# Performance work log

Hardware: AMD Instinct MI355X
Metric: run time of the kernel (lower is better)

The kernel has to match this reference:

```python
import jax, jax.numpy as jnp
import numpy as np

G, NP, K, H, DH, D, NL = 256, 1000, 8, 8, 10, 80, 10  # graphs, nodes/graph, knn, heads, d_head, hidden, layers


def setup_inputs() -> dict:
    key = jax.random.key(0)
    ks = jax.random.split(key, 16)
    rn = lambda k, shape: (jax.random.normal(k, shape, jnp.float32) * 0.05)
    return dict(
        h_feat=jax.random.normal(ks[0], (G, NP, 9), jnp.float32),
        bn_gamma=jnp.ones((9,), jnp.float32), bn_beta=jnp.zeros((9,), jnp.float32),
        W_emb=rn(ks[1], (9, D)), b_emb=jnp.zeros((D,), jnp.float32),
        Wq=rn(ks[2], (NL, D, D)), Wk=rn(ks[3], (NL, D, D)), Wv=rn(ks[4], (NL, D, D)),
        Wo=rn(ks[5], (NL, D, D)), bo=jnp.zeros((NL, D), jnp.float32),
        W1=rn(ks[6], (NL, D, 2 * D)), b1=jnp.zeros((NL, 2 * D), jnp.float32),
        W2=rn(ks[7], (NL, 2 * D, D)), b2=jnp.zeros((NL, D), jnp.float32),
        Wr0=rn(ks[8], (D, 40)), br0=jnp.zeros((40,), jnp.float32),
        Wr1=rn(ks[9], (40, 20)), br1=jnp.zeros((20,), jnp.float32),
        Wr2=rn(ks[10], (20, 64)), br2=jnp.zeros((64,), jnp.float32),
        W_clust=rn(ks[11], (64, 3)),
        W_beta=rn(ks[12], (64, 1)), b_beta=jnp.zeros((1,), jnp.float32),
    )


def _forward(h_feat, bn_gamma, bn_beta, W_emb, b_emb, Wq, Wk, Wv, Wo, bo,
             W1, b1, W2, b2, Wr0, br0, Wr1, br1, Wr2, br2, W_clust, W_beta, b_beta):
    # knn graph on raw coords (first 3 feature columns), per graph, k=8 (self included)
    coords = h_feat[..., :3]
    d2 = jnp.sum((coords[:, :, None, :] - coords[:, None, :, :]) ** 2, -1)  # [G,NP,NP]
    nbr = jax.lax.top_k(-d2, K)[1]  # [G,NP,K] neighbor indices per destination node
    gidx = jnp.arange(G)[:, None, None]

    # BatchNorm1d (training-mode batch stats over all nodes) + embedding
    x = h_feat.reshape(-1, 9)
    mu = x.mean(0)
    var = x.var(0)
    x = (x - mu) / jnp.sqrt(var + 1e-5) * bn_gamma + bn_beta
    h = (x @ W_emb + b_emb).reshape(G, NP, D)

    inv_sqrt_d = jnp.float32(1.0 / np.sqrt(DH))

    def layer(h, p):
        wq, wk, wv, wo, bo_, w1, b1_, w2, b2_ = p
        q = (h @ wq).reshape(G, NP, H, DH)
        k_ = (h @ wk).reshape(G, NP, H, DH)
        v = (h @ wv).reshape(G, NP, H, DH)
        kn = k_[gidx, nbr]  # [G,NP,K,H,DH] gather src K over edges
        vn = v[gidx, nbr]
        s = jnp.einsum('gnkhd,gnhd->gnkh', kn, q) * inv_sqrt_d
        s = jnp.exp(jnp.clip(s, -5.0, 5.0))  # scaled_exp with clamp
        wV = jnp.einsum('gnkh,gnkhd->gnhd', s, vn)
        attn = (wV / (s.sum(2)[..., None] + 1e-6)).reshape(G, NP, D)
        h = h + attn @ wo + bo_  # O proj + residual (no LN/BN)
        h = h + jax.nn.relu(h @ w1 + b1_) @ w2 + b2_  # FFN + residual
        return h, None

    h, _ = jax.lax.scan(layer, h, (Wq, Wk, Wv, Wo, bo, W1, b1, W2, b2))

    # MLPReadout 80->40->20->64 (ReLU between), then clustering coords + beta
    y = h.reshape(-1, D)
    y = jax.nn.relu(y @ Wr0 + br0)
    y = jax.nn.relu(y @ Wr1 + br1)
    y = y @ Wr2 + br2
    cc = y @ W_clust  # [N,3], no bias
    beta = y @ W_beta + b_beta  # [N,1]
    return jnp.concatenate([cc, beta], axis=1)  # [N,4]


def reference(h_feat, bn_gamma, bn_beta, W_emb, b_emb, Wq, Wk, Wv, Wo, bo,
              W1, b1, W2, b2, Wr0, br0, Wr1, br1, Wr2, br2, W_clust, W_beta, b_beta):
    return _forward(h_feat, bn_gamma, bn_beta, W_emb, b_emb, Wq, Wk, Wv, Wo, bo,
                    W1, b1, W2, b2, Wr0, br0, Wr1, br1, Wr2, br2, W_clust, W_beta, b_beta)
```

## Files before the change

### kernel.cpp

```cpp
#include <hip/hip_runtime.h>
#include <cstdint>
#include <cstddef>


typedef __attribute__((ext_vector_type(8))) short short8v;
typedef __attribute__((ext_vector_type(4))) float f32x4;

#define MFMA16(ACC, A, B) ACC = __builtin_amdgcn_mfma_f32_16x16x32_bf16(A, B, ACC, 0, 0, 0)
#define MF3(ACC, AH, AL, BH, BL) { MFMA16(ACC, AH, BH); MFMA16(ACC, AH, BL); MFMA16(ACC, AL, BH); }

__device__ __forceinline__ void splitbf(float x, unsigned short& hi, unsigned short& lo) {
  unsigned u = __float_as_uint(x);
  unsigned r = u + 0x7FFFu + ((u >> 16) & 1u);
  hi = (unsigned short)(r >> 16);
  float hf = __uint_as_float(((unsigned)hi) << 16);
  float lf = x - hf;
  unsigned u2 = __float_as_uint(lf);
  unsigned r2 = u2 + 0x7FFFu + ((u2 >> 16) & 1u);
  lo = (unsigned short)(r2 >> 16);
}

__device__ __forceinline__ float bf2f(unsigned short v) {
  return __uint_as_float(((unsigned)v) << 16);
}

__global__ __launch_bounds__(128) void knn_kernel(const float* __restrict__ hf, int* __restrict__ nbr) {
  __shared__ __align__(16) float cs[3000];
  int b = blockIdx.x;
  int g = b >> 3;
  int q = b & 7;
  for (int i = threadIdx.x; i < 3000; i += 128) {
    cs[i] = hf[((size_t)g * 1000 + (i / 3)) * 9 + (i % 3)];
  }
  __syncthreads();
  int tid = threadIdx.x;
  if (tid < 125) {
    int n = q * 125 + tid;
    float cx = cs[n * 3 + 0], cy = cs[n * 3 + 1], cz = cs[n * 3 + 2];
    float bd[8];
    int bi[8];
    #pragma unroll
    for (int q2 = 0; q2 < 8; ++q2) { bd[q2] = 3.402823466e38f; bi[q2] = 0; }
    for (int j = 0; j < 1000; j += 4) {
      float4 a = *reinterpret_cast<const float4*>(cs + j * 3);
      float4 b4 = *reinterpret_cast<const float4*>(cs + j * 3 + 4);
      float4 c4 = *reinterpret_cast<const float4*>(cs + j * 3 + 8);
      float d2v[4];
      {
        float dx = __fsub_rn(cx, a.x), dy = __fsub_rn(cy, a.y), dz = __fsub_rn(cz, a.z);
        d2v[0] = __fadd_rn(__fadd_rn(__fmul_rn(dx, dx), __fmul_rn(dy, dy)), __fmul_rn(dz, dz));
      }
      {
        float dx = __fsub_rn(cx, a.w), dy = __fsub_rn(cy, b4.x), dz = __fsub_rn(cz, b4.y);
        d2v[1] = __fadd_rn(__fadd_rn(__fmul_rn(dx, dx), __fmul_rn(dy, dy)), __fmul_rn(dz, dz));
      }
      {
        float dx = __fsub_rn(cx, b4.z), dy = __fsub_rn(cy, b4.w), dz = __fsub_rn(cz, c4.x);
        d2v[2] = __fadd_rn(__fadd_rn(__fmul_rn(dx, dx), __fmul_rn(dy, dy)), __fmul_rn(dz, dz));
      }
      {
        float dx = __fsub_rn(cx, c4.y), dy = __fsub_rn(cy, c4.z), dz = __fsub_rn(cz, c4.w);
        d2v[3] = __fadd_rn(__fadd_rn(__fmul_rn(dx, dx), __fmul_rn(dy, dy)), __fmul_rn(dz, dz));
      }
      #pragma unroll
      for (int u = 0; u < 4; ++u) {
        float d2 = d2v[u];
        if (d2 < bd[7]) {
          bd[7] = d2; bi[7] = j + u;
          #pragma unroll
          for (int q2 = 7; q2 >= 1; --q2) {
            if (bd[q2] < bd[q2 - 1]) {
              float tf = bd[q2]; bd[q2] = bd[q2 - 1]; bd[q2 - 1] = tf;
              int ti = bi[q2]; bi[q2] = bi[q2 - 1]; bi[q2 - 1] = ti;
            }
          }
        }
      }
    }
    #pragma unroll
    for (int kk = 0; kk < 8; ++kk) nbr[((size_t)g * 1000 + n) * 8 + kk] = bi[kk];
  }
}

__global__ __launch_bounds__(256) void bn_stat1(const float* __restrict__ hf, float* __restrict__ partial) {
  __shared__ float red[4][18];
  int row = blockIdx.x * 256 + threadIdx.x;
  float s[9], ss[9];
  #pragma unroll
  for (int f = 0; f < 9; ++f) {
    float v = hf[(size_t)row * 9 + f];
    s[f] = v;
    ss[f] = v * v;
  }
  for (int off = 32; off > 0; off >>= 1) {
    #pragma unroll
    for (int f = 0; f < 9; ++f) {
      s[f] += __shfl_down(s[f], off);
      ss[f] += __shfl_down(ss[f], off);
    }
  }
  int wid = threadIdx.x >> 6, lane = threadIdx.x & 63;
  if (lane == 0) {
    #pragma unroll
    for (int f = 0; f < 9; ++f) { red[wid][f] = s[f]; red[wid][9 + f] = ss[f]; }
  }
  __syncthreads();
  if (threadIdx.x < 18) {
    partial[(size_t)blockIdx.x * 18 + threadIdx.x] =
        red[0][threadIdx.x] + red[1][threadIdx.x] + red[2][threadIdx.x] + red[3][threadIdx.x];
  }
}

__global__ __launch_bounds__(256) void bn_stat2(const float* __restrict__ partial, float* __restrict__ stats) {
  __shared__ double sd[9][28], qd[9][28];
  int tid = threadIdx.x;
  if (tid < 252) {
    int f = tid % 9, gq = tid / 9;
    double s = 0.0, q = 0.0;
    for (int b = gq; b < 1000; b += 28) {
      s += (double)partial[b * 18 + f];
      q += (double)partial[b * 18 + 9 + f];
    }
    sd[f][gq] = s;
    qd[f][gq] = q;
  }
  __syncthreads();
  if (tid < 9) {
    double s = 0.0, q = 0.0;
    for (int g2 = 0; g2 < 28; ++g2) { s += sd[tid][g2]; q += qd[tid][g2]; }
    double mu = s / 256000.0;
    double var = q / 256000.0 - mu * mu;
    stats[tid] = (float)mu;
    stats[9 + tid] = (float)(1.0 / sqrt(var + 1e-5));
  }
}

__global__ __launch_bounds__(256) void split_tr(const float* __restrict__ src, unsigned short* __restrict__ dhi,
                                                unsigned short* __restrict__ dlo, int R, int C, int KS) {
  const float* s = src + (size_t)blockIdx.x * R * C;
  unsigned short* dh = dhi + (size_t)blockIdx.x * C * KS;
  unsigned short* dl = dlo + (size_t)blockIdx.x * C * KS;
  int n = C * KS;
  for (int i = threadIdx.x; i < n; i += 256) {
    int c = i / KS, kk = i % KS;
    float v = (kk < R) ? s[kk * C + c] : 0.f;
    unsigned short h, l;
    splitbf(v, h, l);
    dh[i] = h;
    dl[i] = l;
  }
}

__global__ __launch_bounds__(320) void embed_kernel(const float* __restrict__ hf, const float* __restrict__ stats,
                                                    const float* __restrict__ gamma, const float* __restrict__ beta,
                                                    const float* __restrict__ We, const float* __restrict__ be,
                                                    float* __restrict__ h) {
  __shared__ __align__(16) float xs[40 * 9];
  size_t p0 = (size_t)blockIdx.x * 40;
  for (int i = threadIdx.x; i < 360; i += 320) {
    int f = i % 9;
    float x = hf[p0 * 9 + i];
    xs[i] = (x - stats[f]) * stats[9 + f] * gamma[f] + beta[f];
  }
  __syncthreads();
  int c = threadIdx.x % 80, pg = threadIdx.x / 80;
  float we[9];
  #pragma unroll
  for (int f = 0; f < 9; ++f) we[f] = We[f * 80 + c];
  float bias = be[c];
  for (int pp = 0; pp < 10; ++pp) {
    int p = pg * 10 + pp;
    float acc = 0.f;
    #pragma unroll
    for (int f = 0; f < 9; ++f) acc = fmaf(xs[p * 9 + f], we[f], acc);
    h[(p0 + p) * 80 + c] = acc + bias;
  }
}

__global__ __launch_bounds__(320) void kv_kernel(const float* __restrict__ h,
                                                 const unsigned short* __restrict__ WkH, const unsigned short* __restrict__ WkL,
                                                 const unsigned short* __restrict__ WvH, const unsigned short* __restrict__ WvL,
                                                 float* __restrict__ kb, float* __restrict__ vb) {
  __shared__ __align__(16) unsigned short ahi[48 * 104];
  __shared__ __align__(16) unsigned short alo[48 * 104];
  size_t p0 = (size_t)blockIdx.x * 40;
  int tid = threadIdx.x;
  int lane = tid & 63, wv = tid >> 6;
  int fr = lane & 15, fq = lane >> 4;
  for (int i = tid; i < 800; i += 320) {
    int row = i / 20, kq = i % 20;
    float4 v = reinterpret_cast<const float4*>(h + (p0 + row) * 80)[kq];
    unsigned short h0, l0, h1, l1, h2, l2, h3, l3;
    splitbf(v.x, h0, l0); splitbf(v.y, h1, l1); splitbf(v.z, h2, l2); splitbf(v.w, h3, l3);
    int off = row * 104 + kq * 4;
    *reinterpret_cast<unsigned*>(&ahi[off]) = (unsigned)h0 | ((unsigned)h1 << 16);
    *reinterpret_cast<unsigned*>(&ahi[off + 2]) = (unsigned)h2 | ((unsigned)h3 << 16);
    *reinterpret_cast<unsigned*>(&alo[off]) = (unsigned)l0 | ((unsigned)l1 << 16);
    *reinterpret_cast<unsigned*>(&alo[off + 2]) = (unsigned)l2 | ((unsigned)l3 << 16);
  }
  for (int i = tid; i < 384; i += 320) {
    int row = i >> 3, kk = 80 + ((i & 7) << 1);
    int off = row * 104 + kk;
    *reinterpret_cast<unsigned*>(&ahi[off]) = 0u;
    *reinterpret_cast<unsigned*>(&alo[off]) = 0u;
  }
  __syncthreads();
  int bcol = wv * 16 + fr;
  f32x4 ck0 = {0.f, 0.f, 0.f, 0.f}, ck1 = ck0, ck2 = ck0;
  f32x4 cv0 = ck0, cv1 = ck0, cv2 = ck0;
  #pragma unroll
  for (int ks = 0; ks < 3; ++ks) {
    int boff = bcol * 96 + ks * 32 + fq * 8;
    short8v bkh = *reinterpret_cast<const short8v*>(WkH + boff);
    short8v bkl = *reinterpret_cast<const short8v*>(WkL + boff);
    short8v bvh = *reinterpret_cast<const short8v*>(WvH + boff);
    short8v bvl = *reinterpret_cast<const short8v*>(WvL + boff);
    int a0 = (0 * 16 + fr) * 104 + ks * 32 + fq * 8;
    int a1 = (1 * 16 + fr) * 104 + ks * 32 + fq * 8;
    int a2 = (2 * 16 + fr) * 104 + ks * 32 + fq * 8;
    short8v ah0 = *reinterpret_cast<const short8v*>(ahi + a0);
    short8v al0 = *reinterpret_cast<const short8v*>(alo + a0);
    MF3(ck0, ah0, al0, bkh, bkl); MF3(cv0, ah0, al0, bvh, bvl);
    short8v ah1 = *reinterpret_cast<const short8v*>(ahi + a1);
    short8v al1 = *reinterpret_cast<const short8v*>(alo + a1);
    MF3(ck1, ah1, al1, bkh, bkl); MF3(cv1, ah1, al1, bvh, bvl);
    short8v ah2 = *reinterpret_cast<const short8v*>(ahi + a2);
    short8v al2 = *reinterpret_cast<const short8v*>(alo + a2);
    MF3(ck2, ah2, al2, bkh, bkl); MF3(cv2, ah2, al2, bvh, bvl);
  }
  #pragma unroll
  for (int j = 0; j < 4; ++j) {
    int r0 = fq * 4 + j;
    kb[(p0 + r0) * 80 + bcol] = ck0[j];
    vb[(p0 + r0) * 80 + bcol] = cv0[j];
    int r1 = 16 + r0;
    kb[(p0 + r1) * 80 + bcol] = ck1[j];
    vb[(p0 + r1) * 80 + bcol] = cv1[j];
    int r2 = 32 + r0;
    if (r2 < 40) {
      kb[(p0 + r2) * 80 + bcol] = ck2[j];
      vb[(p0 + r2) * 80 + bcol] = cv2[j];
    }
  }
}

__global__ __launch_bounds__(320) void battn_kernel(const float* __restrict__ h, const float* __restrict__ kb,
                                                    const float* __restrict__ vb, const int* __restrict__ nbr,
                                                    const unsigned short* __restrict__ WqH, const unsigned short* __restrict__ WqL,
                                                    const unsigned short* __restrict__ WoH, const unsigned short* __restrict__ WoL,
                                                    const float* __restrict__ bo,
                                                    const unsigned short* __restrict__ W1H, const unsigned short* __restrict__ W1L,
                                                    const float* __restrict__ b1,
                                                    const unsigned short* __restrict__ W2H, const unsigned short* __restrict__ W2L,
                                                    const float* __restrict__ b2, float* __restrict__ hout) {
  __shared__ __align__(16) unsigned short ahi[48 * 168];
  __shared__ __align__(16) unsigned short alo[48 * 168];
  int b = blockIdx.x;
  int xcd = b & 7;
  int r = b >> 3;
  int graph = (xcd << 5) + (r / 25);
  int jb = r % 25;
  size_t gbase = (size_t)graph * 1000;
  size_t pbase = gbase + (size_t)jb * 40;
  int tid = threadIdx.x;
  int lane = tid & 63, wv = tid >> 6;
  int fr = lane & 15, fq = lane >> 4;
  int pA = tid >> 3, hhA = tid & 7;
  int nb[8];
  #pragma unroll
  for (int kk = 0; kk < 8; ++kk) nb[kk] = nbr[(pbase + pA) * 8 + kk];
  for (int i = tid; i < 800; i += 320) {
    int row = i / 20, kq = i % 20;
    float4 v = reinterpret_cast<const float4*>(h + (pbase + row) * 80)[kq];
    unsigned short h0, l0, h1, l1, h2_, l2, h3, l3;
    splitbf(v.x, h0, l0); splitbf(v.y, h1, l1); splitbf(v.z, h2_, l2); splitbf(v.w, h3, l3);
    int off = row * 168 + kq * 4;
    *reinterpret_cast<unsigned*>(&ahi[off]) = (unsigned)h0 | ((unsigned)h1 << 16);
    *reinterpret_cast<unsigned*>(&ahi[off + 2]) = (unsigned)h2_ | ((unsigned)h3 << 16);
    *reinterpret_cast<unsigned*>(&alo[off]) = (unsigned)l0 | ((unsigned)l1 << 16);
    *reinterpret_cast<unsigned*>(&alo[off + 2]) = (unsigned)l2 | ((unsigned)l3 << 16);
  }
  for (int i = tid; i < 384; i += 320) {
    int row = i >> 3, kk = 80 + ((i & 7) << 1);
    int off = row * 168 + kk;
    *reinterpret_cast<unsigned*>(&ahi[off]) = 0u;
    *reinterpret_cast<unsigned*>(&alo[off]) = 0u;
  }
  __syncthreads();
  int bcol = wv * 16 + fr;
  f32x4 q0 = {0.f, 0.f, 0.f, 0.f}, q1 = q0, q2 = q0;
  {
    #pragma unroll
    for (int ks = 0; ks < 3; ++ks) {
      int boff = bcol * 96 + ks * 32 + fq * 8;
      short8v bh = *reinterpret_cast<const short8v*>(WqH + boff);
      short8v bl = *reinterpret_cast<const short8v*>(WqL + boff);
      int a0 = (0 * 16 + fr) * 168 + ks * 32 + fq * 8;
      int a1 = (1 * 16 + fr) * 168 + ks * 32 + fq * 8;
      int a2 = (2 * 16 + fr) * 168 + ks * 32 + fq * 8;
      short8v ah0 = *reinterpret_cast<const short8v*>(ahi + a0);
      short8v al0 = *reinterpret_cast<const short8v*>(alo + a0);
      MF3(q0, ah0, al0, bh, bl);
      short8v ah1 = *reinterpret_cast<const short8v*>(ahi + a1);
      short8v al1 = *reinterpret_cast<const short8v*>(alo + a1);
      MF3(q1, ah1, al1, bh, bl);
      short8v ah2 = *reinterpret_cast<const short8v*>(ahi + a2);
      short8v al2 = *reinterpret_cast<const short8v*>(alo + a2);
      MF3(q2, ah2, al2, bh, bl);
    }
  }
  __syncthreads();
  {
    #pragma unroll
    for (int j = 0; j < 4; ++j) {
      unsigned short hh_, ll_;
      int r0 = fq * 4 + j;
      splitbf(q0[j], hh_, ll_);
      ahi[r0 * 168 + bcol] = hh_; alo[r0 * 168 + bcol] = ll_;
      int r1 = 16 + r0;
      splitbf(q1[j], hh_, ll_);
      ahi[r1 * 168 + bcol] = hh_; alo[r1 * 168 + bcol] = ll_;
      int r2 = 32 + r0;
      if (r2 < 40) {
        splitbf(q2[j], hh_, ll_);
        ahi[r2 * 168 + bcol] = hh_; alo[r2 * 168 + bcol] = ll_;
      }
    }
  }
  __syncthreads();
  {
    int p = pA, hh = hhA;
    float qv[10];
    #pragma unroll
    for (int d2 = 0; d2 < 5; ++d2) {
      int off = p * 168 + hh * 10 + 2 * d2;
      unsigned uh = *reinterpret_cast<const unsigned*>(&ahi[off]);
      unsigned ul = *reinterpret_cast<const unsigned*>(&alo[off]);
      qv[2 * d2] = bf2f((unsigned short)uh) + bf2f((unsigned short)ul);
      qv[2 * d2 + 1] = bf2f((unsigned short)(uh >> 16)) + bf2f((unsigned short)(ul >> 16));
    }
    float sv[8];
    float denom = 0.f;
    #pragma unroll
    for (int kk = 0; kk < 8; ++kk) {
      const float2* kr = reinterpret_cast<const float2*>(kb + (gbase + nb[kk]) * 80 + hh * 10);
      float acc = 0.f;
      #pragma unroll
      for (int d2 = 0; d2 < 5; ++d2) {
        float2 kv2 = kr[d2];
        acc = fmaf(qv[2 * d2], kv2.x, acc);
        acc = fmaf(qv[2 * d2 + 1], kv2.y, acc);
      }
      float s = acc * 0.31622776601683794f;
      s = fminf(fmaxf(s, -5.f), 5.f);
      s = expf(s);
      sv[kk] = s;
      denom += s;
    }
    float wV[10] = {0, 0, 0, 0, 0, 0, 0, 0, 0, 0};
    #pragma unroll
    for (int kk = 0; kk < 8; ++kk) {
      const float2* vr = reinterpret_cast<const float2*>(vb + (gbase + nb[kk]) * 80 + hh * 10);
      #pragma unroll
      for (int d2 = 0; d2 < 5; ++d2) {
        float2 vv = vr[d2];
        wV[2 * d2] = fmaf(sv[kk], vv.x, wV[2 * d2]);
        wV[2 * d2 + 1] = fmaf(sv[kk], vv.y, wV[2 * d2 + 1]);
      }
    }
    float dn = denom + 1e-6f;
    #pragma unroll
    for (int d2 = 0; d2 < 5; ++d2) {
      float x0 = wV[2 * d2] / dn;
      float x1 = wV[2 * d2 + 1] / dn;
      unsigned short h0, l0, h1, l1;
      splitbf(x0, h0, l0); splitbf(x1, h1, l1);
      int off = p * 168 + hh * 10 + 2 * d2;
      *reinterpret_cast<unsigned*>(&ahi[off]) = (unsigned)h0 | ((unsigned)h1 << 16);
      *reinterpret_cast<unsigned*>(&alo[off]) = (unsigned)l0 | ((unsigned)l1 << 16);
    }
  }
  __syncthreads();
  f32x4 o0 = {0.f, 0.f, 0.f, 0.f}, o1 = o0, o2 = o0;
  {
    #pragma unroll
    for (int ks = 0; ks < 3; ++ks) {
      int boff = bcol * 96 + ks * 32 + fq * 8;
      short8v bh = *reinterpret_cast<const short8v*>(WoH + boff);
      short8v bl = *reinterpret_cast<const short8v*>(WoL + boff);
      int a0 = (0 * 16 + fr) * 168 + ks * 32 + fq * 8;
      int a1 = (1 * 16 + fr) * 168 + ks * 32 + fq * 8;
      int a2 = (2 * 16 + fr) * 168 + ks * 32 + fq * 8;
      short8v ah0 = *reinterpret_cast<const short8v*>(ahi + a0);
      short8v al0 = *reinterpret_cast<const short8v*>(alo + a0);
      MF3(o0, ah0, al0, bh, bl);
      short8v ah1 = *reinterpret_cast<const short8v*>(ahi + a1);
      short8v al1 = *reinterpret_cast<const short8v*>(alo + a1);
      MF3(o1, ah1, al1, bh, bl);
      short8v ah2 = *reinterpret_cast<const short8v*>(ahi + a2);
      short8v al2 = *reinterpret_cast<const short8v*>(alo + a2);
      MF3(o2, ah2, al2, bh, bl);
    }
  }
  __syncthreads();
  {
    float bias = bo[bcol];
    #pragma unroll
    for (int j = 0; j < 4; ++j) {
      unsigned short hh_, ll_;
      int r0 = fq * 4 + j;
      o0[j] = h[(pbase + r0) * 80 + bcol] + o0[j] + bias;
      splitbf(o0[j], hh_, ll_);
      ahi[r0 * 168 + bcol] = hh_; alo[r0 * 168 + bcol] = ll_;
      int r1 = 16 + r0;
      o1[j] = h[(pbase + r1) * 80 + bcol] + o1[j] + bias;
      splitbf(o1[j], hh_, ll_);
      ahi[r1 * 168 + bcol] = hh_; alo[r1 * 168 + bcol] = ll_;
      int r2 = 32 + r0;
      if (r2 < 40) {
        o2[j] = h[(pbase + r2) * 80 + bcol] + o2[j] + bias;
        splitbf(o2[j], hh_, ll_);
        ahi[r2 * 168 + bcol] = hh_; alo[r2 * 168 + bcol] = ll_;
      }
    }
  }
  __syncthreads();
  f32x4 t00 = {0.f, 0.f, 0.f, 0.f}, t01 = t00, t02 = t00;
  f32x4 t10 = t00, t11 = t00, t12 = t00;
  {
    int bc0 = wv * 16 + fr, bc1 = (wv + 5) * 16 + fr;
    #pragma unroll
    for (int ks = 0; ks < 3; ++ks) {
      int b0 = bc0 * 96 + ks * 32 + fq * 8;
      int b1o = bc1 * 96 + ks * 32 + fq * 8;
      short8v bh0 = *reinterpret_cast<const short8v*>(W1H + b0);
      short8v bl0 = *reinterpret_cast<const short8v*>(W1L + b0);
      short8v bh1 = *reinterpret_cast<const short8v*>(W1H + b1o);
      short8v bl1 = *reinterpret_cast<const short8v*>(W1L + b1o);
      int a0 = (0 * 16 + fr) * 168 + ks * 32 + fq * 8;
      int a1 = (1 * 16 + fr) * 168 + ks * 32 + fq * 8;
      int a2 = (2 * 16 + fr) * 168 + ks * 32 + fq * 8;
      short8v ah0 = *reinterpret_cast<const short8v*>(ahi + a0);
      short8v al0 = *reinterpret_cast<const short8v*>(alo + a0);
      MF3(t00, ah0, al0, bh0, bl0); MF3(t10, ah0, al0, bh1, bl1);
      short8v ah1 = *reinterpret_cast<const short8v*>(ahi + a1);
      short8v al1 = *reinterpret_cast<const short8v*>(alo + a1);
      MF3(t01, ah1, al1, bh0, bl0); MF3(t11, ah1, al1, bh1, bl1);
      short8v ah2 = *reinterpret_cast<const short8v*>(ahi + a2);
      short8v al2 = *reinterpret_cast<const short8v*>(alo + a2);
      MF3(t02, ah2, al2, bh0, bl0); MF3(t12, ah2, al2, bh1, bl1);
    }
  }
  __syncthreads();
  {
    int bc0 = wv * 16 + fr, bc1 = (wv + 5) * 16 + fr;
    float bias0 = b1[bc0], bias1 = b1[bc1];
    #pragma unroll
    for (int j = 0; j < 4; ++j) {
      unsigned short hh_, ll_;
      int r0 = fq * 4 + j;
      float t = fmaxf(t00[j] + bias0, 0.f);
      splitbf(t, hh_, ll_); ahi[r0 * 168 + bc0] = hh_; alo[r0 * 168 + bc0] = ll_;
      t = fmaxf(t10[j] + bias1, 0.f);
      splitbf(t, hh_, ll_); ahi[r0 * 168 + bc1] = hh_; alo[r0 * 168 + bc1] = ll_;
      int r1 = 16 + r0;
      t = fmaxf(t01[j] + bias0, 0.f);
      splitbf(t, hh_, ll_); ahi[r1 * 168 + bc0] = hh_; alo[r1 * 168 + bc0] = ll_;
      t = fmaxf(t11[j] + bias1, 0.f);
      splitbf(t, hh_, ll_); ahi[r1 * 168 + bc1] = hh_; alo[r1 * 168 + bc1] = ll_;
      int r2 = 32 + r0;
      if (r2 < 40) {
        t = fmaxf(t02[j] + bias0, 0.f);
        splitbf(t, hh_, ll_); ahi[r2 * 168 + bc0] = hh_; alo[r2 * 168 + bc0] = ll_;
        t = fmaxf(t12[j] + bias1, 0.f);
        splitbf(t, hh_, ll_); ahi[r2 * 168 + bc1] = hh_; alo[r2 * 168 + bc1] = ll_;
      }
    }
  }
  __syncthreads();
  {
    f32x4 c0 = {0.f, 0.f, 0.f, 0.f}, c1 = c0, c2 = c0;
    #pragma unroll
    for (int ks = 0; ks < 5; ++ks) {
      int boff = bcol * 160 + ks * 32 + fq * 8;
      short8v bh = *reinterpret_cast<const short8v*>(W2H + boff);
      short8v bl = *reinterpret_cast<const short8v*>(W2L + boff);
      int a0 = (0 * 16 + fr) * 168 + ks * 32 + fq * 8;
      int a1 = (1 * 16 + fr) * 168 + ks * 32 + fq * 8;
      int a2 = (2 * 16 + fr) * 168 + ks * 32 + fq * 8;
      short8v ah0 = *reinterpret_cast<const short8v*>(ahi + a0);
      short8v al0 = *reinterpret_cast<const short8v*>(alo + a0);
      MF3(c0, ah0, al0, bh, bl);
      short8v ah1 = *reinterpret_cast<const short8v*>(ahi + a1);
      short8v al1 = *reinterpret_cast<const short8v*>(alo + a1);
      MF3(c1, ah1, al1, bh, bl);
      short8v ah2 = *reinterpret_cast<const short8v*>(ahi + a2);
      short8v al2 = *reinterpret_cast<const short8v*>(alo + a2);
      MF3(c2, ah2, al2, bh, bl);
    }
    float bias = b2[bcol];
    #pragma unroll
    for (int j = 0; j < 4; ++j) {
      int r0 = fq * 4 + j;
      hout[(pbase + r0) * 80 + bcol] = o0[j] + c0[j] + bias;
      int r1 = 16 + r0;
      hout[(pbase + r1) * 80 + bcol] = o1[j] + c1[j] + bias;
      int r2 = 32 + r0;
      if (r2 < 40) hout[(pbase + r2) * 80 + bcol] = o2[j] + c2[j] + bias;
    }
  }
}

__global__ __launch_bounds__(320) void readout_kernel(const float* __restrict__ h, const float* __restrict__ Wr0,
                                                      const float* __restrict__ br0, const float* __restrict__ Wr1,
                                                      const float* __restrict__ br1, const float* __restrict__ Wr2,
                                                      const float* __restrict__ br2, const float* __restrict__ Wc,
                                                      const float* __restrict__ Wb, const float* __restrict__ bb,
                                                      float* __restrict__ out) {
  __shared__ __align__(16) float hs[3200];
  __shared__ __align__(16) float y0s[40 * 40];
  __shared__ __align__(16) float y1s[40 * 20];
  __shared__ __align__(16) float y2s[40 * 64];
  size_t p0 = (size_t)blockIdx.x * 40;
  int tid = threadIdx.x;
  {
    const float4* src = reinterpret_cast<const float4*>(h + p0 * 80);
    float4* dst = reinterpret_cast<float4*>(hs);
    for (int i = tid; i < 800; i += 320) dst[i] = src[i];
  }
  __syncthreads();
  {
    int c = tid % 40, grp = tid / 40;
    if (grp < 5) {
      float wcol[80];
      #pragma unroll
      for (int kk = 0; kk < 80; ++kk) wcol[kk] = Wr0[kk * 40 + c];
      float bias = br0[c];
      float acc[8] = {};
      #pragma unroll
      for (int j = 0; j < 8; ++j) {
        const float4* r4 = reinterpret_cast<const float4*>(hs + (grp * 8 + j) * 80);
        #pragma unroll
        for (int kq = 0; kq < 20; ++kq) {
          float4 hv = r4[kq];
          acc[j] = fmaf(hv.x, wcol[4 * kq + 0], acc[j]);
          acc[j] = fmaf(hv.y, wcol[4 * kq + 1], acc[j]);
          acc[j] = fmaf(hv.z, wcol[4 * kq + 2], acc[j]);
          acc[j] = fmaf(hv.w, wcol[4 * kq + 3], acc[j]);
        }
      }
      #pragma unroll
      for (int j = 0; j < 8; ++j) y0s[(grp * 8 + j) * 40 + c] = fmaxf(acc[j] + bias, 0.f);
    }
  }
  __syncthreads();
  {
    int c = tid % 20, grp = tid / 20;
    if (grp < 5) {
      float wcol[40];
      #pragma unroll
      for (int kk = 0; kk < 40; ++kk) wcol[kk] = Wr1[kk * 20 + c];
      float bias = br1[c];
      float acc[8] = {};
      #pragma unroll
      for (int j = 0; j < 8; ++j) {
        const float4* r4 = reinterpret_cast<const float4*>(y0s + (grp * 8 + j) * 40);
        #pragma unroll
        for (int kq = 0; kq < 10; ++kq) {
          float4 hv = r4[kq];
          acc[j] = fmaf(hv.x, wcol[4 * kq + 0], acc[j]);
          acc[j] = fmaf(hv.y, wcol[4 * kq + 1], acc[j]);
          acc[j] = fmaf(hv.z, wcol[4 * kq + 2], acc[j]);
          acc[j] = fmaf(hv.w, wcol[4 * kq + 3], acc[j]);
        }
      }
      #pragma unroll
      for (int j = 0; j < 8; ++j) y1s[(grp * 8 + j) * 20 + c] = fmaxf(acc[j] + bias, 0.f);
    }
  }
  __syncthreads();
  {
    int c = tid % 64, grp = tid / 64;
    float wcol[20];
    #pragma unroll
    for (int kk = 0; kk < 20; ++kk) wcol[kk] = Wr2[kk * 64 + c];
    float bias = br2[c];
    float acc[8] = {};
    #pragma unroll
    for (int j = 0; j < 8; ++j) {
      const float4* r4 = reinterpret_cast<const float4*>(y1s + (grp * 8 + j) * 20);
      #pragma unroll
      for (int kq = 0; kq < 5; ++kq) {
        float4 hv = r4[kq];
        acc[j] = fmaf(hv.x, wcol[4 * kq + 0], acc[j]);
        acc[j] = fmaf(hv.y, wcol[4 * kq + 1], acc[j]);
        acc[j] = fmaf(hv.z, wcol[4 * kq + 2], acc[j]);
        acc[j] = fmaf(hv.w, wcol[4 * kq + 3], acc[j]);
      }
    }
    #pragma unroll
    for (int j = 0; j < 8; ++j) y2s[(grp * 8 + j) * 64 + c] = acc[j] + bias;
  }
  __syncthreads();
  {
    int c = tid % 4, p = tid / 4;
    if (p < 40) {
      float wcol[64];
      if (c < 3) {
        #pragma unroll
        for (int kk = 0; kk < 64; ++kk) wcol[kk] = Wc[kk * 3 + c];
      } else {
        #pragma unroll
        for (int kk = 0; kk < 64; ++kk) wcol[kk] = Wb[kk];
      }
      float acc = 0.f;
      #pragma unroll
      for (int kk = 0; kk < 64; ++kk) acc = fmaf(y2s[p * 64 + kk], wcol[kk], acc);
      if (c == 3) acc += bb[0];
      out[(p0 + p) * 4 + c] = acc;
    }
  }
}

extern "C" void kernel_launch(void* const* d_in, const int* in_sizes, int n_in,
                              void* d_out, int out_size, void* d_ws, size_t ws_size,
                              hipStream_t stream) {
  const float* hf = (const float*)d_in[0];
  const float* gamma = (const float*)d_in[1];
  const float* beta = (const float*)d_in[2];
  const float* We = (const float*)d_in[3];
  const float* be = (const float*)d_in[4];
  const float* Wq = (const float*)d_in[5];
  const float* Wk = (const float*)d_in[6];
  const float* Wv = (const float*)d_in[7];
  const float* Wo = (const float*)d_in[8];
  const float* bo = (const float*)d_in[9];
  const float* W1 = (const float*)d_in[10];
  const float* b1 = (const float*)d_in[11];
  const float* W2 = (const float*)d_in[12];
  const float* b2 = (const float*)d_in[13];
  const float* Wr0 = (const float*)d_in[14];
  const float* br0 = (const float*)d_in[15];
  const float* Wr1 = (const float*)d_in[16];
  const float* br1 = (const float*)d_in[17];
  const float* Wr2 = (const float*)d_in[18];
  const float* br2 = (const float*)d_in[19];
  const float* Wc = (const float*)d_in[20];
  const float* Wb = (const float*)d_in[21];
  const float* bb = (const float*)d_in[22];
  float* out = (float*)d_out;

  char* wsp = (char*)d_ws;
  int* nbr = (int*)wsp;            wsp += (size_t)256000 * 8 * 4;
  float* hA = (float*)wsp;         wsp += (size_t)256000 * 80 * 4;
  float* kbuf = (float*)wsp;       wsp += (size_t)256000 * 80 * 4;
  float* vbuf = (float*)wsp;       wsp += (size_t)256000 * 80 * 4;
  float* partial = (float*)wsp;    wsp += (size_t)1000 * 18 * 4;
  float* stats = (float*)wsp;      wsp += 128;
  unsigned short* WqH = (unsigned short*)wsp; wsp += (size_t)10 * 7680 * 2;
  unsigned short* WqL = (unsigned short*)wsp; wsp += (size_t)10 * 7680 * 2;
  unsigned short* WkH = (unsigned short*)wsp; wsp += (size_t)10 * 7680 * 2;
  unsigned short* WkL = (unsigned short*)wsp; wsp += (size_t)10 * 7680 * 2;
  unsigned short* WvH = (unsigned short*)wsp; wsp += (size_t)10 * 7680 * 2;
  unsigned short* WvL = (unsigned short*)wsp; wsp += (size_t)10 * 7680 * 2;
  unsigned short* WoH = (unsigned short*)wsp; wsp += (size_t)10 * 7680 * 2;
  unsigned short* WoL = (unsigned short*)wsp; wsp += (size_t)10 * 7680 * 2;
  unsigned short* W1H = (unsigned short*)wsp; wsp += (size_t)10 * 15360 * 2;
  unsigned short* W1L = (unsigned short*)wsp; wsp += (size_t)10 * 15360 * 2;
  unsigned short* W2H = (unsigned short*)wsp; wsp += (size_t)10 * 12800 * 2;
  unsigned short* W2L = (unsigned short*)wsp; wsp += (size_t)10 * 12800 * 2;

  knn_kernel<<<2048, 128, 0, stream>>>(hf, nbr);
  bn_stat1<<<1000, 256, 0, stream>>>(hf, partial);
  bn_stat2<<<1, 256, 0, stream>>>(partial, stats);
  split_tr<<<10, 256, 0, stream>>>(Wq, WqH, WqL, 80, 80, 96);
  split_tr<<<10, 256, 0, stream>>>(Wk, WkH, WkL, 80, 80, 96);
  split_tr<<<10, 256, 0, stream>>>(Wv, WvH, WvL, 80, 80, 96);
  split_tr<<<10, 256, 0, stream>>>(Wo, WoH, WoL, 80, 80, 96);
  split_tr<<<10, 256, 0, stream>>>(W1, W1H, W1L, 80, 160, 96);
  split_tr<<<10, 256, 0, stream>>>(W2, W2H, W2L, 160, 80, 160);
  embed_kernel<<<6400, 320, 0, stream>>>(hf, stats, gamma, beta, We, be, hA);
  for (int l = 0; l < 10; ++l) {
    kv_kernel<<<6400, 320, 0, stream>>>(hA, WkH + (size_t)l * 7680, WkL + (size_t)l * 7680,
                                        WvH + (size_t)l * 7680, WvL + (size_t)l * 7680, kbuf, vbuf);
    battn_kernel<<<6400, 320, 0, stream>>>(hA, kbuf, vbuf, nbr,
                                           WqH + (size_t)l * 7680, WqL + (size_t)l * 7680,
                                           WoH + (size_t)l * 7680, WoL + (size_t)l * 7680, bo + (size_t)l * 80,
                                           W1H + (size_t)l * 15360, W1L + (size_t)l * 15360, b1 + (size_t)l * 160,
                                           W2H + (size_t)l * 12800, W2L + (size_t)l * 12800, b2 + (size_t)l * 80, hA);
  }
  readout_kernel<<<6400, 320, 0, stream>>>(hA, Wr0, br0, Wr1, br1, Wr2, br2, Wc, Wb, bb, out);
}
```

Measured before the change: 3.568 ms.

## Give each wave its own 16-row tile in battn so the dense GEMMs skip block barriers

The fused attention+FFN kernel now handles 80 nodes per block instead of 40, and each of the 5 waves owns a private 16-row stripe and computes all output columns for it. The Q, O, W1 and W2 projections therefore only touch that wave's rows of shared memory, which removes most __syncthreads (only two remain around the cross-row neighbour attention). Each thread handles two nodes in the attention step. This halves the grid and the per-block overhead, at the cost of more accumulator registers (up to 10 f32x4 tiles), more weight loads per wave, and a 40-row tail block per graph with masked rows.

Measured after the change: 4.502 ms. 26.2% more time.

```diff
diff --git a/kernel.cpp b/kernel.cpp
--- a/kernel.cpp
+++ b/kernel.cpp
@@ -244,6 +244,60 @@
   }
 }
 
+__device__ __forceinline__ void attn_point(int p, int hh, const int* __restrict__ nb, size_t gbase,
+                                           const float* __restrict__ kb, const float* __restrict__ vb,
+                                           unsigned short* __restrict__ ahi, unsigned short* __restrict__ alo) {
+  float qv[10];
+  #pragma unroll
+  for (int d2 = 0; d2 < 5; ++d2) {
+    int off = p * 168 + hh * 10 + 2 * d2;
+    unsigned uh = *reinterpret_cast<const unsigned*>(&ahi[off]);
+    unsigned ul = *reinterpret_cast<const unsigned*>(&alo[off]);
+    qv[2 * d2] = bf2f((unsigned short)uh) + bf2f((unsigned short)ul);
+    qv[2 * d2 + 1] = bf2f((unsigned short)(uh >> 16)) + bf2f((unsigned short)(ul >> 16));
+  }
+  float sv[8];
+  float denom = 0.f;
+  #pragma unroll
+  for (int kk = 0; kk < 8; ++kk) {
+    const float2* kr = reinterpret_cast<const float2*>(kb + (gbase + nb[kk]) * 80 + hh * 10);
+    float acc = 0.f;
+    #pragma unroll
+    for (int d2 = 0; d2 < 5; ++d2) {
+      float2 kv2 = kr[d2];
+      acc = fmaf(qv[2 * d2], kv2.x, acc);
+      acc = fmaf(qv[2 * d2 + 1], kv2.y, acc);
+    }
+    float s = acc * 0.31622776601683794f;
+    s = fminf(fmaxf(s, -5.f), 5.f);
+    s = expf(s);
+    sv[kk] = s;
+    denom += s;
+  }
+  float wV[10] = {0, 0, 0, 0, 0, 0, 0, 0, 0, 0};
+  #pragma unroll
+  for (int kk = 0; kk < 8; ++kk) {
+    const float2* vr = reinterpret_cast<const float2*>(vb + (gbase + nb[kk]) * 80 + hh * 10);
+    #pragma unroll
+    for (int d2 = 0; d2 < 5; ++d2) {
+      float2 vv = vr[d2];
+      wV[2 * d2] = fmaf(sv[kk], vv.x, wV[2 * d2]);
+      wV[2 * d2 + 1] = fmaf(sv[kk], vv.y, wV[2 * d2 + 1]);
+    }
+  }
+  float dn = denom + 1e-6f;
+  #pragma unroll
+  for (int d2 = 0; d2 < 5; ++d2) {
+    float x0 = wV[2 * d2] / dn;
+    float x1 = wV[2 * d2 + 1] / dn;
+    unsigned short h0, l0, h1, l1;
+    splitbf(x0, h0, l0); splitbf(x1, h1, l1);
+    int off = p * 168 + hh * 10 + 2 * d2;
+    *reinterpret_cast<unsigned*>(&ahi[off]) = (unsigned)h0 | ((unsigned)h1 << 16);
+    *reinterpret_cast<unsigned*>(&alo[off]) = (unsigned)l0 | ((unsigned)l1 << 16);
+  }
+}
+
 __global__ __launch_bounds__(320) void battn_kernel(const float* __restrict__ h, const float* __restrict__ kb,
                                                     const float* __restrict__ vb, const int* __restrict__ nbr,
                                                     const unsigned short* __restrict__ WqH, const unsigned short* __restrict__ WqL,
@@ -253,25 +307,37 @@
                                                     const float* __restrict__ b1,
                                                     const unsigned short* __restrict__ W2H, const unsigned short* __restrict__ W2L,
                                                     const float* __restrict__ b2, float* __restrict__ hout) {
-  __shared__ __align__(16) unsigned short ahi[48 * 168];
-  __shared__ __align__(16) unsigned short alo[48 * 168];
+  __shared__ __align__(16) unsigned short ahi[80 * 168];
+  __shared__ __align__(16) unsigned short alo[80 * 168];
   int b = blockIdx.x;
   int xcd = b & 7;
   int r = b >> 3;
-  int graph = (xcd << 5) + (r / 25);
-  int jb = r % 25;
+  int graph = (xcd << 5) + (r / 13);
+  int t = r % 13;
   size_t gbase = (size_t)graph * 1000;
-  size_t pbase = gbase + (size_t)jb * 40;
+  size_t pbase = gbase + (size_t)t * 80;
+  int nrows = (t == 12) ? 40 : 80;
   int tid = threadIdx.x;
   int lane = tid & 63, wv = tid >> 6;
   int fr = lane & 15, fq = lane >> 4;
-  int pA = tid >> 3, hhA = tid & 7;
-  int nb[8];
-  #pragma unroll
-  for (int kk = 0; kk < 8; ++kk) nb[kk] = nbr[(pbase + pA) * 8 + kk];
-  for (int i = tid; i < 800; i += 320) {
-    int row = i / 20, kq = i % 20;
-    float4 v = reinterpret_cast<const float4*>(h + (pbase + row) * 80)[kq];
+  int rowbase = wv * 16;
+  int p1 = tid >> 3, hh = tid & 7;
+  int p2 = p1 + 40;
+  bool has2 = p2 < nrows;
+  int nb1[8], nb2[8];
+  #pragma unroll
+  for (int kk = 0; kk < 8; ++kk) nb1[kk] = nbr[(pbase + p1) * 8 + kk];
+  if (has2) {
+    #pragma unroll
+    for (int kk = 0; kk < 8; ++kk) nb2[kk] = nbr[(pbase + p2) * 8 + kk];
+  }
+  #pragma unroll
+  for (int s = 0; s < 5; ++s) {
+    int i = lane + 64 * s;
+    int rl = i / 20, kq = i % 20;
+    int row = rowbase + rl;
+    float4 v = {0.f, 0.f, 0.f, 0.f};
+    if (row < nrows) v = reinterpret_cast<const float4*>(h + (pbase + row) * 80)[kq];
     unsigned short h0, l0, h1, l1, h2_, l2, h3, l3;
     splitbf(v.x, h0, l0); splitbf(v.y, h1, l1); splitbf(v.z, h2_, l2); splitbf(v.w, h3, l3);
     int off = row * 168 + kq * 4;
@@ -280,233 +346,132 @@
     *reinterpret_cast<unsigned*>(&alo[off]) = (unsigned)l0 | ((unsigned)l1 << 16);
     *reinterpret_cast<unsigned*>(&alo[off + 2]) = (unsigned)l2 | ((unsigned)l3 << 16);
   }
-  for (int i = tid; i < 384; i += 320) {
-    int row = i >> 3, kk = 80 + ((i & 7) << 1);
+  #pragma unroll
+  for (int s = 0; s < 2; ++s) {
+    int i = lane + 64 * s;
+    int row = rowbase + (i >> 3);
+    int kk = 80 + ((i & 7) << 1);
     int off = row * 168 + kk;
     *reinterpret_cast<unsigned*>(&ahi[off]) = 0u;
     *reinterpret_cast<unsigned*>(&alo[off]) = 0u;
   }
-  __syncthreads();
-  int bcol = wv * 16 + fr;
-  f32x4 q0 = {0.f, 0.f, 0.f, 0.f}, q1 = q0, q2 = q0;
-  {
+  {
+    f32x4 C[5] = {};
     #pragma unroll
     for (int ks = 0; ks < 3; ++ks) {
-      int boff = bcol * 96 + ks * 32 + fq * 8;
-      short8v bh = *reinterpret_cast<const short8v*>(WqH + boff);
-      short8v bl = *reinterpret_cast<const short8v*>(WqL + boff);
-      int a0 = (0 * 16 + fr) * 168 + ks * 32 + fq * 8;
-      int a1 = (1 * 16 + fr) * 168 + ks * 32 + fq * 8;
-      int a2 = (2 * 16 + fr) * 168 + ks * 32 + fq * 8;
-      short8v ah0 = *reinterpret_cast<const short8v*>(ahi + a0);
-      short8v al0 = *reinterpret_cast<const short8v*>(alo + a0);
-      MF3(q0, ah0, al0, bh, bl);
-      short8v ah1 = *reinterpret_cast<const short8v*>(ahi + a1);
-      short8v al1 = *reinterpret_cast<const short8v*>(alo + a1);
-      MF3(q1, ah1, al1, bh, bl);
-      short8v ah2 = *reinterpret_cast<const short8v*>(ahi + a2);
-      short8v al2 = *reinterpret_cast<const short8v*>(alo + a2);
-      MF3(q2, ah2, al2, bh, bl);
-    }
-  }
-  __syncthreads();
-  {
-    #pragma unroll
-    for (int j = 0; j < 4; ++j) {
-      unsigned short hh_, ll_;
-      int r0 = fq * 4 + j;
-      splitbf(q0[j], hh_, ll_);
-      ahi[r0 * 168 + bcol] = hh_; alo[r0 * 168 + bcol] = ll_;
-      int r1 = 16 + r0;
-      splitbf(q1[j], hh_, ll_);
-      ahi[r1 * 168 + bcol] = hh_; alo[r1 * 168 + bcol] = ll_;
-      int r2 = 32 + r0;
-      if (r2 < 40) {
-        splitbf(q2[j], hh_, ll_);
-        ahi[r2 * 168 + bcol] = hh_; alo[r2 * 168 + bcol] = ll_;
-      }
-    }
-  }
-  __syncthreads();
-  {
-    int p = pA, hh = hhA;
-    float qv[10];
-    #pragma unroll
-    for (int d2 = 0; d2 < 5; ++d2) {
-      int off = p * 168 + hh * 10 + 2 * d2;
-      unsigned uh = *reinterpret_cast<const unsigned*>(&ahi[off]);
-      unsigned ul = *reinterpret_cast<const unsigned*>(&alo[off]);
-      qv[2 * d2] = bf2f((unsigned short)uh) + bf2f((unsigned short)ul);
-      qv[2 * d2 + 1] = bf2f((unsigned short)(uh >> 16)) + bf2f((unsigned short)(ul >> 16));
-    }
-    float sv[8];
-    float denom = 0.f;
-    #pragma unroll
-    for (int kk = 0; kk < 8; ++kk) {
-      const float2* kr = reinterpret_cast<const float2*>(kb + (gbase + nb[kk]) * 80 + hh * 10);
-      float acc = 0.f;
-      #pragma unroll
-      for (int d2 = 0; d2 < 5; ++d2) {
-        float2 kv2 = kr[d2];
-        acc = fmaf(qv[2 * d2], kv2.x, acc);
-        acc = fmaf(qv[2 * d2 + 1], kv2.y, acc);
-      }
-      float s = acc * 0.31622776601683794f;
-      s = fminf(fmaxf(s, -5.f), 5.f);
-      s = expf(s);
-      sv[kk] = s;
-      denom += s;
-    }
-    float wV[10] = {0, 0, 0, 0, 0, 0, 0, 0, 0, 0};
-    #pragma unroll
-    for (int kk = 0; kk < 8; ++kk) {
-      const float2* vr = reinterpret_cast<const float2*>(vb + (gbase + nb[kk]) * 80 + hh * 10);
-      #pragma unroll
-      for (int d2 = 0; d2 < 5; ++d2) {
-        float2 vv = vr[d2];
-        wV[2 * d2] = fmaf(sv[kk], vv.x, wV[2 * d2]);
-        wV[2 * d2 + 1] = fmaf(sv[kk], vv.y, wV[2 * d2 + 1]);
-      }
-    }
-    float dn = denom + 1e-6f;
-    #pragma unroll
-    for (int d2 = 0; d2 < 5; ++d2) {
-      float x0 = wV[2 * d2] / dn;
-      float x1 = wV[2 * d2 + 1] / dn;
-      unsigned short h0, l0, h1, l1;
-      splitbf(x0, h0, l0); splitbf(x1, h1, l1);
-      int off = p * 168 + hh * 10 + 2 * d2;
-      *reinterpret_cast<unsigned*>(&ahi[off]) = (unsigned)h0 | ((unsigned)h1 << 16);
-      *reinterpret_cast<unsigned*>(&alo[off]) = (unsigned)l0 | ((unsigned)l1 << 16);
-    }
-  }
-  __syncthreads();
-  f32x4 o0 = {0.f, 0.f, 0.f, 0.f}, o1 = o0, o2 = o0;
+      int aoff = (rowbase + fr) * 168 + ks * 32 + fq * 8;
+      short8v ah = *reinterpret_cast<const short8v*>(ahi + aoff);
+      short8v al = *reinterpret_cast<const short8v*>(alo + aoff);
+      #pragma unroll
+      for (int ct = 0; ct < 5; ++ct) {
+        int boff = (ct * 16 + fr) * 96 + ks * 32 + fq * 8;
+        short8v bh = *reinterpret_cast<const short8v*>(WqH + boff);
+        short8v bl = *reinterpret_cast<const short8v*>(WqL + boff);
+        MF3(C[ct], ah, al, bh, bl);
+      }
+    }
+    #pragma unroll
+    for (int ct = 0; ct < 5; ++ct) {
+      int col = ct * 16 + fr;
+      #pragma unroll
+      for (int j = 0; j < 4; ++j) {
+        int row = rowbase + fq * 4 + j;
+        unsigned short hh_, ll_;
+        splitbf(C[ct][j], hh_, ll_);
+        ahi[row * 168 + col] = hh_;
+        alo[row * 168 + col] = ll_;
+      }
+    }
+  }
+  __syncthreads();
+  attn_point(p1, hh, nb1, gbase, kb, vb, ahi, alo);
+  if (has2) attn_point(p2, hh, nb2, gbase, kb, vb, ahi, alo);
+  __syncthreads();
+  f32x4 O[5] = {};
   {
     #pragma unroll
     for (int ks = 0; ks < 3; ++ks) {
-      int boff = bcol * 96 + ks * 32 + fq * 8;
-      short8v bh = *reinterpret_cast<const short8v*>(WoH + boff);
-      short8v bl = *reinterpret_cast<const short8v*>(WoL + boff);
-      int a0 = (0 * 16 + fr) * 168 + ks * 32 + fq * 8;
-      int a1 = (1 * 16 + fr) * 168 + ks * 32 + fq * 8;
-      int a2 = (2 * 16 + fr) * 168 + ks * 32 + fq * 8;
-      short8v ah0 = *reinterpret_cast<const short8v*>(ahi + a0);
-      short8v al0 = *reinterpret_cast<const short8v*>(alo + a0);
-      MF3(o0, ah0, al0, bh, bl);
-      short8v ah1 = *reinterpret_cast<const short8v*>(ahi + a1);
-      short8v al1 = *reinterpret_cast<const short8v*>(alo + a1);
-      MF3(o1, ah1, al1, bh, bl);
-      short8v ah2 = *reinterpret_cast<const short8v*>(ahi + a2);
-      short8v al2 = *reinterpret_cast<const short8v*>(alo + a2);
-      MF3(o2, ah2, al2, bh, bl);
-    }
-  }
-  __syncthreads();
-  {
-    float bias = bo[bcol];
-    #pragma unroll
-    for (int j = 0; j < 4; ++j) {
-      unsigned short hh_, ll_;
-      int r0 = fq * 4 + j;
-      o0[j] = h[(pbase + r0) * 80 + bcol] + o0[j] + bias;
-      splitbf(o0[j], hh_, ll_);
-      ahi[r0 * 168 + bcol] = hh_; alo[r0 * 168 + bcol] = ll_;
-      int r1 = 16 + r0;
-      o1[j] = h[(pbase + r1) * 80 + bcol] + o1[j] + bias;
-      splitbf(o1[j], hh_, ll_);
-      ahi[r1 * 168 + bcol] = hh_; alo[r1 * 168 + bcol] = ll_;
-      int r2 = 32 + r0;
-      if (r2 < 40) {
-        o2[j] = h[(pbase + r2) * 80 + bcol] + o2[j] + bias;
-        splitbf(o2[j], hh_, ll_);
-        ahi[r2 * 168 + bcol] = hh_; alo[r2 * 168 + bcol] = ll_;
-      }
-    }
-  }
-  __syncthreads();
-  f32x4 t00 = {0.f, 0.f, 0.f, 0.f}, t01 = t00, t02 = t00;
-  f32x4 t10 = t00, t11 = t00, t12 = t00;
-  {
-    int bc0 = wv * 16 + fr, bc1 = (wv + 5) * 16 + fr;
+      int aoff = (rowbase + fr) * 168 + ks * 32 + fq * 8;
+      short8v ah = *reinterpret_cast<const short8v*>(ahi + aoff);
+      short8v al = *reinterpret_cast<const short8v*>(alo + aoff);
+      #pragma unroll
+      for (int ct = 0; ct < 5; ++ct) {
+        int boff = (ct * 16 + fr) * 96 + ks * 32 + fq * 8;
+        short8v bh = *reinterpret_cast<const short8v*>(WoH + boff);
+        short8v bl = *reinterpret_cast<const short8v*>(WoL + boff);
+        MF3(O[ct], ah, al, bh, bl);
+      }
+    }
+    #pragma unroll
+    for (int ct = 0; ct < 5; ++ct) {
+      int col = ct * 16 + fr;
+      float bias = bo[col];
+      #pragma unroll
+      for (int j = 0; j < 4; ++j) {
+        int row = rowbase + fq * 4 + j;
+        float hv = (row < nrows) ? h[(pbase + row) * 80 + col] : 0.f;
+        O[ct][j] = hv + O[ct][j] + bias;
+        unsigned short hh_, ll_;
+        splitbf(O[ct][j], hh_, ll_);
+        ahi[row * 168 + col] = hh_;
+        alo[row * 168 + col] = ll_;
+      }
+    }
+  }
+  {
+    f32x4 T[10] = {};
     #pragma unroll
     for (int ks = 0; ks < 3; ++ks) {
-      int b0 = bc0 * 96 + ks * 32 + fq * 8;
-      int b1o = bc1 * 96 + ks * 32 + fq * 8;
-      short8v bh0 = *reinterpret_cast<const short8v*>(W1H + b0);
-      short8v bl0 = *reinterpret_cast<const short8v*>(W1L + b0);
-      short8v bh1 = *reinterpret_cast<const short8v*>(W1H + b1o);
-      short8v bl1 = *reinterpret_cast<const short8v*>(W1L + b1o);
-      int a0 = (0 * 16 + fr) * 168 + ks * 32 + fq * 8;
-      int a1 = (1 * 16 + fr) * 168 + ks * 32 + fq * 8;
-      int a2 = (2 * 16 + fr) * 168 + ks * 32 + fq * 8;
-      short8v ah0 = *reinterpret_cast<const short8v*>(ahi + a0);
-      short8v al0 = *reinterpret_cast<const short8v*>(alo + a0);
-      MF3(t00, ah0, al0, bh0, bl0); MF3(t10, ah0, al0, bh1, bl1);
-      short8v ah1 = *reinterpret_cast<const short8v*>(ahi + a1);
-      short8v al1 = *reinterpret_cast<const short8v*>(alo + a1);
-      MF3(t01, ah1, al1, bh0, bl0); MF3(t11, ah1, al1, bh1, bl1);
-      short8v ah2 = *reinterpret_cast<const short8v*>(ahi + a2);
-      short8v al2 = *reinterpret_cast<const short8v*>(alo + a2);
-      MF3(t02, ah2, al2, bh0, bl0); MF3(t12, ah2, al2, bh1, bl1);
-    }
-  }
-  __syncthreads();
-  {
-    int bc0 = wv * 16 + fr, bc1 = (wv + 5) * 16 + fr;
-    float bias0 = b1[bc0], bias1 = b1[bc1];
-    #pragma unroll
-    for (int j = 0; j < 4; ++j) {
-      unsigned short hh_, ll_;
-      int r0 = fq * 4 + j;
-      float t = fmaxf(t00[j] + bias0, 0.f);
-      splitbf(t, hh_, ll_); ahi[r0 * 168 + bc0] = hh_; alo[r0 * 168 + bc0] = ll_;
-      t = fmaxf(t10[j] + bias1, 0.f);
-      splitbf(t, hh_, ll_); ahi[r0 * 168 + bc1] = hh_; alo[r0 * 168 + bc1] = ll_;
-      int r1 = 16 + r0;
-      t = fmaxf(t01[j] + bias0, 0.f);
-      splitbf(t, hh_, ll_); ahi[r1 * 168 + bc0] = hh_; alo[r1 * 168 + bc0] = ll_;
-      t = fmaxf(t11[j] + bias1, 0.f);
-      splitbf(t, hh_, ll_); ahi[r1 * 168 + bc1] = hh_; alo[r1 * 168 + bc1] = ll_;
-      int r2 = 32 + r0;
-      if (r2 < 40) {
-        t = fmaxf(t02[j] + bias0, 0.f);
-        splitbf(t, hh_, ll_); ahi[r2 * 168 + bc0] = hh_; alo[r2 * 168 + bc0] = ll_;
-        t = fmaxf(t12[j] + bias1, 0.f);
-        splitbf(t, hh_, ll_); ahi[r2 * 168 + bc1] = hh_; alo[r2 * 168 + bc1] = ll_;
-      }
-    }
-  }
-  __syncthreads();
-  {
-    f32x4 c0 = {0.f, 0.f, 0.f, 0.f}, c1 = c0, c2 = c0;
+      int aoff = (rowbase + fr) * 168 + ks * 32 + fq * 8;
+      short8v ah = *reinterpret_cast<const short8v*>(ahi + aoff);
+      short8v al = *reinterpret_cast<const short8v*>(alo + aoff);
+      #pragma unroll
+      for (int ct = 0; ct < 10; ++ct) {
+        int boff = (ct * 16 + fr) * 96 + ks * 32 + fq * 8;
+        short8v bh = *reinterpret_cast<const short8v*>(W1H + boff);
+        short8v bl = *reinterpret_cast<const short8v*>(W1L + boff);
+        MF3(T[ct], ah, al, bh, bl);
+      }
+    }
+    #pragma unroll
+    for (int ct = 0; ct < 10; ++ct) {
+      int col = ct * 16 + fr;
+      float bias = b1[col];
+      #pragma unroll
+      for (int j = 0; j < 4; ++j) {
+        int row = rowbase + fq * 4 + j;
+        float tv = fmaxf(T[ct][j] + bias, 0.f);
+        unsigned short hh_, ll_;
+        splitbf(tv, hh_, ll_);
+        ahi[row * 168 + col] = hh_;
+        alo[row * 168 + col] = ll_;
+      }
+    }
+  }
+  {
+    f32x4 D[5] = {};
     #pragma unroll
     for (int ks = 0; ks < 5; ++ks) {
-      int boff = bcol * 160 + ks * 32 + fq * 8;
-      short8v bh = *reinterpret_cast<const short8v*>(W2H + boff);
-      short8v bl = *reinterpret_cast<const short8v*>(W2L + boff);
-      int a0 = (0 * 16 + fr) * 168 + ks * 32 + fq * 8;
-      int a1 = (1 * 16 + fr) * 168 + ks * 32 + fq * 8;
-      int a2 = (2 * 16 + fr) * 168 + ks * 32 + fq * 8;
-      short8v ah0 = *reinterpret_cast<const short8v*>(ahi + a0);
-      short8v al0 = *reinterpret_cast<const short8v*>(alo + a0);
-      MF3(c0, ah0, al0, bh, bl);
-      short8v ah1 = *reinterpret_cast<const short8v*>(ahi + a1);
-      short8v al1 = *reinterpret_cast<const short8v*>(alo + a1);
-      MF3(c1, ah1, al1, bh, bl);
-      short8v ah2 = *reinterpret_cast<const short8v*>(ahi + a2);
-      short8v al2 = *reinterpret_cast<const short8v*>(alo + a2);
-      MF3(c2, ah2, al2, bh, bl);
-    }
-    float bias = b2[bcol];
-    #pragma unroll
-    for (int j = 0; j < 4; ++j) {
-      int r0 = fq * 4 + j;
-      hout[(pbase + r0) * 80 + bcol] = o0[j] + c0[j] + bias;
-      int r1 = 16 + r0;
-      hout[(pbase + r1) * 80 + bcol] = o1[j] + c1[j] + bias;
-      int r2 = 32 + r0;
-      if (r2 < 40) hout[(pbase + r2) * 80 + bcol] = o2[j] + c2[j] + bias;
+      int aoff = (rowbase + fr) * 168 + ks * 32 + fq * 8;
+      short8v ah = *reinterpret_cast<const short8v*>(ahi + aoff);
+      short8v al = *reinterpret_cast<const short8v*>(alo + aoff);
+      #pragma unroll
+      for (int ct = 0; ct < 5; ++ct) {
+        int boff = (ct * 16 + fr) * 160 + ks * 32 + fq * 8;
+        short8v bh = *reinterpret_cast<const short8v*>(W2H + boff);
+        short8v bl = *reinterpret_cast<const short8v*>(W2L + boff);
+        MF3(D[ct], ah, al, bh, bl);
+      }
+    }
+    #pragma unroll
+    for (int ct = 0; ct < 5; ++ct) {
+      int col = ct * 16 + fr;
+      float bias = b2[col];
+      #pragma unroll
+      for (int j = 0; j < 4; ++j) {
+        int row = rowbase + fq * 4 + j;
+        if (row < nrows) hout[(pbase + row) * 80 + col] = O[ct][j] + D[ct][j] + bias;
+      }
     }
   }
 }
@@ -683,7 +648,7 @@
   for (int l = 0; l < 10; ++l) {
     kv_kernel<<<6400, 320, 0, stream>>>(hA, WkH + (size_t)l * 7680, WkL + (size_t)l * 7680,
                                         WvH + (size_t)l * 7680, WvL + (size_t)l * 7680, kbuf, vbuf);
-    battn_kernel<<<6400, 320, 0, stream>>>(hA, kbuf, vbuf, nbr,
+    battn_kernel<<<3328, 320, 0, stream>>>(hA, kbuf, vbuf, nbr,
                                            WqH + (size_t)l * 7680, WqL + (size_t)l * 7680,
                                            WoH + (size_t)l * 7680, WoL + (size_t)l * 7680, bo + (size_t)l * 80,
                                            W1H + (size_t)l * 15360, W1L + (size_t)l * 15360, b1 + (size_t)l * 160,
```
